# Kernel tuning notes

Hardware: AMD Instinct MI355X
Metric: run time of the kernel (lower is better)

The kernel has to match this reference:

```python
import jax, jax.numpy as jnp
import numpy as np

N = 100000      # n_nodes
D = 64          # in_features (= out_features)
H = 4           # attention heads
DK = D // H     # per-head dim
E = 1600000     # num edges (avg degree 16)
STEP = 0.25     # ODE euler step size
NSTEPS = 4      # integrate t in [0, 1]
ALPHA = 0.2     # LeakyReLU negative slope


def setup_inputs() -> dict:
    key = jax.random.key(0)
    k1, k2, k3, k4 = jax.random.split(key, 4)
    x = jax.random.normal(k1, (N, D), dtype=jnp.float32)
    edge_index = jax.random.randint(k2, (2, E), 0, N, dtype=jnp.int32)
    edge_weight = jax.random.uniform(k3, (E,), dtype=jnp.float32)
    # HamAgg.weight: init.eye_ -> identity [D, D]
    W = jnp.eye(D, dtype=jnp.float32)
    # HAM_GATConv.a: xavier_normal_ on shape (2*d_k, 1, 1), gain=1.414
    a = jax.random.normal(k4, (2 * DK,), dtype=jnp.float32) * (1.414 * np.sqrt(2.0 / (2 * DK + 1)))
    return {"x": x, "edge_index": edge_index, "edge_weight": edge_weight, "W": W, "a": a}


def reference(x, edge_index, edge_weight, W, a):
    # ---- Hamiltonian ODE block (args.vt == 'fc', odemap 'h1extend') ----
    # xt = hstack([x, x @ W.T]); euler-integrate canonical Hamiltonian flow
    # dq/dt = p, dp/dt = -q over t in [0,1] with step 0.25; keep first D dims.
    q = x
    p = x @ W.T
    for _ in range(NSTEPS):
        q, p = q + STEP * p, p - STEP * q
    xt = q  # out_x = out[..., :D]

    row, col = edge_index[0], edge_index[1]

    # ---- HAM_GATConv attention (W_x = x @ I = x) ----
    # h[n, head, k] = xt[n, head*DK + k]
    h = xt.reshape(N, H, DK)
    a_src, a_dst = a[:DK], a[DK:]
    s_src = h @ a_src   # [N, H] per-node source contribution
    s_dst = h @ a_dst   # [N, H] per-node dest contribution
    score = jax.nn.leaky_relu(s_src[row] + s_dst[col], ALPHA)  # [E, H]

    # segment softmax grouped by destination (edge[1])
    seg_max = jax.ops.segment_max(score, col, num_segments=N)  # [N, H]
    seg_max = jnp.where(jnp.isfinite(seg_max), seg_max, 0.0)
    e = jnp.exp(score - seg_max[col])
    denom = jax.ops.segment_sum(e, col, num_segments=N)
    att = e / (denom[col] + 1e-16)  # [E, H]

    # ---- mean over heads of per-head spmm == single spmm with mean attention ----
    # spmm: out[row[e]] += att[e] * xt[col[e]]
    w = att.mean(axis=1)  # [E]
    out = jax.ops.segment_sum(w[:, None] * xt[col], row, num_segments=N)  # [N, D]
    return out
```

## Files before the change

### kernel.cpp

```cpp
#include <hip/hip_runtime.h>
#include <hip/hip_bf16.h>


#define LRELU(v) ((v) > 0.0f ? (v) : 0.2f * (v))

#define EC 4096
#define BSC 256
#define BSR 128
#define NPW 8
#define NPB 32
#define SLOTS 4

__device__ __forceinline__ float bf16_to_f32(unsigned short u) {
    return __uint_as_float((unsigned int)u << 16);
}
__device__ __forceinline__ float bflo(unsigned int u) {
    return __uint_as_float(u << 16);
}
__device__ __forceinline__ float bfhi(unsigned int u) {
    return __uint_as_float(u & 0xFFFF0000u);
}
__device__ __forceinline__ unsigned short f32_to_bf16(float f) {
    __hip_bfloat16 h = __float2bfloat16(f);
    return *reinterpret_cast<unsigned short*>(&h);
}

__global__ __launch_bounds__(256) void k_node(const float* __restrict__ x,
                                              const float* __restrict__ W,
                                              const float* __restrict__ a,
                                              unsigned short* __restrict__ xt16,
                                              float* __restrict__ s_src,
                                              float* __restrict__ s_dst,
                                              int n, float c1, float c2) {
    __shared__ float Ws[64 * 68];
    __shared__ float xs[NPB * 64];
    int t = threadIdx.x;
    for (int i = t; i < 64 * 64; i += 256)
        Ws[(i >> 6) * 68 + (i & 63)] = W[i];
    {
        size_t gbase = (size_t)blockIdx.x * NPB * 64;
        for (int i = t; i < NPB * 64; i += 256) {
            size_t g = gbase + i;
            xs[i] = (g < (size_t)n * 64) ? x[g] : 0.0f;
        }
    }
    __syncthreads();
    int wave = t >> 6;
    int lane = t & 63;
    float a_s = a[lane & 15];
    float a_d = a[16 + (lane & 15)];
    int nbase = blockIdx.x * NPB + wave * NPW;
    const float* xw = xs + wave * NPW * 64;

    float p[NPW];
#pragma unroll
    for (int j = 0; j < NPW; ++j) p[j] = 0.0f;

#pragma unroll 2
    for (int k4 = 0; k4 < 64; k4 += 4) {
        float4 wr = *(const float4*)(Ws + lane * 68 + k4);
#pragma unroll
        for (int j = 0; j < NPW; ++j) {
            float4 xb = *(const float4*)(xw + j * 64 + k4);
            p[j] = fmaf(xb.x, wr.x, p[j]);
            p[j] = fmaf(xb.y, wr.y, p[j]);
            p[j] = fmaf(xb.z, wr.z, p[j]);
            p[j] = fmaf(xb.w, wr.w, p[j]);
        }
    }

#pragma unroll
    for (int j = 0; j < NPW; ++j) {
        int node = nbase + j;
        if (node < n) {
            float xv = xw[j * 64 + lane];
            float xtv = c1 * xv + c2 * p[j];
            xt16[(size_t)node * 64 + lane] = f32_to_bf16(xtv);
            float ss = xtv * a_s;
            float sd = xtv * a_d;
#pragma unroll
            for (int off = 8; off >= 1; off >>= 1) {
                ss += __shfl_xor(ss, off, 64);
                sd += __shfl_xor(sd, off, 64);
            }
            if ((lane & 15) == 0) {
                int h = lane >> 4;
                s_src[node * 4 + h] = ss;
                s_dst[node * 4 + h] = sd;
            }
        }
    }
}

__global__ __launch_bounds__(256) void k_hist(const int* __restrict__ row,
                                              const int* __restrict__ col,
                                              int* __restrict__ Hr,
                                              int* __restrict__ Hc,
                                              int e, int nblk, int nbr, int nbc) {
    __shared__ int hr[1024];
    __shared__ int hc[512];
    int t = threadIdx.x;
    for (int i = t; i < 1024; i += 256) hr[i] = 0;
    for (int i = t; i < 512; i += 256) hc[i] = 0;
    __syncthreads();
    int base = blockIdx.x * EC;
#pragma unroll
    for (int j = 0; j < EC / 256; ++j) {
        int i = base + t + j * 256;
        if (i < e) {
            atomicAdd(&hr[row[i] >> 7], 1);
            atomicAdd(&hc[col[i] >> 8], 1);
        }
    }
    __syncthreads();
    for (int b = t; b < nbr; b += 256) Hr[(size_t)b * nblk + blockIdx.x] = hr[b];
    for (int b = t; b < nbc; b += 256) Hc[(size_t)b * nblk + blockIdx.x] = hc[b];
}

__global__ __launch_bounds__(256) void k_scanH2(int* __restrict__ Hr,
                                                int* __restrict__ Hc,
                                                int* __restrict__ BtotR,
                                                int* __restrict__ BtotC,
                                                int nblk, int nbr) {
    __shared__ int vals[512];
    __shared__ int part[256];
    int t = threadIdx.x;
    int bb = blockIdx.x;
    int* Hb;
    int* Btot;
    if (bb < nbr) {
        Hb = Hr + (size_t)bb * nblk;
        Btot = BtotR + bb;
    } else {
        Hb = Hc + (size_t)(bb - nbr) * nblk;
        Btot = BtotC + (bb - nbr);
    }
    for (int i = t; i < nblk; i += 256) vals[i] = Hb[i];
    __syncthreads();
    int c0 = t * 2;
    int s = 0;
#pragma unroll
    for (int j = 0; j < 2; ++j)
        if (c0 + j < nblk) s += vals[c0 + j];
    part[t] = s;
    __syncthreads();
    for (int d = 1; d < 256; d <<= 1) {
        int add = (t >= d) ? part[t - d] : 0;
        __syncthreads();
        part[t] += add;
        __syncthreads();
    }
    int run = part[t] - s;
#pragma unroll
    for (int j = 0; j < 2; ++j) {
        int i = c0 + j;
        if (i < nblk) {
            int v = vals[i];
            Hb[i] = run;
            run += v;
        }
    }
    if (t == 255) *Btot = part[255];
}

__global__ __launch_bounds__(256) void k_base2(const int* __restrict__ BtotR,
                                               int* __restrict__ BbR, int nbr,
                                               const int* __restrict__ BtotC,
                                               int* __restrict__ BbC, int nbc) {
    const int* Btot = (blockIdx.x == 0) ? BtotR : BtotC;
    int* Bbase = (blockIdx.x == 0) ? BbR : BbC;
    int nb = (blockIdx.x == 0) ? nbr : nbc;
    __shared__ int part[256];
    __shared__ int carry;
    int t = threadIdx.x;
    if (t == 0) carry = 0;
    __syncthreads();
    for (int base = 0; base < nb; base += 256) {
        int i = base + t;
        int v = (i < nb) ? Btot[i] : 0;
        part[t] = v;
        __syncthreads();
        for (int d = 1; d < 256; d <<= 1) {
            int add = (t >= d) ? part[t - d] : 0;
            __syncthreads();
            part[t] += add;
            __syncthreads();
        }
        if (i < nb) Bbase[i] = carry + part[t] - v;
        __syncthreads();
        if (t == 0) carry += part[255];
        __syncthreads();
    }
    if (t == 0) Bbase[nb] = carry;
}

__global__ __launch_bounds__(256) void k_scatter_dual(
    const int* __restrict__ row, const int* __restrict__ col,
    const int* __restrict__ Hr, const int* __restrict__ Hc,
    const int* __restrict__ BbR, const int* __restrict__ BbC,
    int* __restrict__ ebr, int* __restrict__ ebc,
    int e, int nblk, int nbr, int nbc) {
    __shared__ int curr[1024];
    __shared__ int curc[512];
    int t = threadIdx.x;
    int blk = blockIdx.x;
    for (int b = t; b < nbr; b += 256) curr[b] = BbR[b] + Hr[(size_t)b * nblk + blk];
    for (int b = t; b < nbc; b += 256) curc[b] = BbC[b] + Hc[(size_t)b * nblk + blk];
    __syncthreads();
    int base = blk * EC;
#pragma unroll
    for (int j = 0; j < EC / 256; ++j) {
        int i = base + t + j * 256;
        if (i < e) {
            int r = row[i], c = col[i];
            int pr = atomicAdd(&curr[r >> 7], 1);
            ebr[pr] = (c << 7) | (r & 127);
            int pc = atomicAdd(&curc[c >> 8], 1);
            ebc[pc] = (r << 8) | (c & 255);
        }
    }
}

__global__ __launch_bounds__(256) void k_denom_b(const int* __restrict__ ebc,
                                                 const int* __restrict__ BbC,
                                                 const float* __restrict__ s_src,
                                                 const float* __restrict__ s_dst,
                                                 float* __restrict__ rden, int n) {
    __shared__ float acc[BSC * 4];
    __shared__ float sd[BSC * 4];
    int t = threadIdx.x;
    int b = blockIdx.x;
    int cbase = b << 8;
    for (int i = t; i < BSC * 4; i += 256) {
        acc[i] = 0.0f;
        int c4 = cbase * 4 + i;
        sd[i] = (c4 < n * 4) ? s_dst[c4] : 0.0f;
    }
    __syncthreads();
    int start = BbC[b], end = BbC[b + 1];
    for (int i = start + t; i < end; i += 256) {
        int p = ebc[i];
        int r = p >> 8, cl = p & 255;
        float4 ss = *(const float4*)(s_src + (size_t)r * 4);
        atomicAdd(&acc[cl * 4 + 0], __expf(LRELU(ss.x + sd[cl * 4 + 0])));
        atomicAdd(&acc[cl * 4 + 1], __expf(LRELU(ss.y + sd[cl * 4 + 1])));
        atomicAdd(&acc[cl * 4 + 2], __expf(LRELU(ss.z + sd[cl * 4 + 2])));
        atomicAdd(&acc[cl * 4 + 3], __expf(LRELU(ss.w + sd[cl * 4 + 3])));
    }
    __syncthreads();
    for (int i = t; i < BSC * 4; i += 256) {
        int c4 = cbase * 4 + i;
        if (c4 < n * 4) rden[c4] = 1.0f / (acc[i] + 1e-16f);
    }
}

__global__ __launch_bounds__(256) void k_sort2(const int* __restrict__ ebr,
                                               const int* __restrict__ BbR,
                                               const float* __restrict__ s_src,
                                               const float* __restrict__ s_dst,
                                               const float* __restrict__ rden,
                                               int* __restrict__ rowptr,
                                               int2* __restrict__ cwp,
                                               int n, int e) {
    __shared__ int cnt[BSR];
    __shared__ int pfx[BSR];
    __shared__ int cur[BSR];
    __shared__ float ssh[BSR * 4];
    int t = threadIdx.x;
    int b = blockIdx.x;
    int rbase = b << 7;
    if (t < BSR) cnt[t] = 0;
    for (int i = t; i < BSR * 4; i += 256) {
        int g = rbase * 4 + i;
        ssh[i] = (g < n * 4) ? s_src[g] : 0.0f;
    }
    __syncthreads();
    int start = BbR[b], end = BbR[b + 1];
    for (int i = start + t; i < end; i += 256)
        atomicAdd(&cnt[ebr[i] & 127], 1);
    __syncthreads();
    if (t < BSR) pfx[t] = cnt[t];
    __syncthreads();
    for (int d = 1; d < BSR; d <<= 1) {
        int v = (t < BSR && t >= d) ? pfx[t - d] : 0;
        __syncthreads();
        if (t < BSR) pfx[t] += v;
        __syncthreads();
    }
    if (t < BSR) {
        int excl = start + pfx[t] - cnt[t];
        cur[t] = excl;
        int r = rbase + t;
        if (r < n) rowptr[r] = excl;
    }
    if (b == 0 && t == 0) rowptr[n] = e;
    __syncthreads();
    for (int i = start + t; i < end; i += 256) {
        int p = ebr[i];
        int rl = p & 127, c = p >> 7;
        float4 sd = *(const float4*)(s_dst + (size_t)c * 4);
        float4 rd = *(const float4*)(rden + (size_t)c * 4);
        float wv = __expf(LRELU(ssh[rl * 4 + 0] + sd.x)) * rd.x +
                   __expf(LRELU(ssh[rl * 4 + 1] + sd.y)) * rd.y +
                   __expf(LRELU(ssh[rl * 4 + 2] + sd.z)) * rd.z +
                   __expf(LRELU(ssh[rl * 4 + 3] + sd.w)) * rd.w;
        int pos = atomicAdd(&cur[rl], 1);
        cwp[pos] = make_int2(c << 6, __float_as_int(0.25f * wv));
    }
}

__global__ __launch_bounds__(256) void k_aggr(const int* __restrict__ rowptr,
                                              const int2* __restrict__ cwp,
                                              const unsigned short* __restrict__ xt16,
                                              float* __restrict__ out, int n, int e) {
    int r = blockIdx.x * 4 + (threadIdx.x >> 6);
    if (r >= n) return;
    int lane = threadIdx.x & 63;
    int g = lane >> 3;
    unsigned le = (lane & 7) << 3;
    int start = rowptr[r], end = rowptr[r + 1];
    float acc[8];
#pragma unroll
    for (int j = 0; j < 8; ++j) acc[j] = 0.0f;
    for (int base = start; base < end; base += SLOTS * 8) {
        int m = end - base;
        if (m > SLOTS * 8) m = SLOTS * 8;
        int nk = (m + 7) >> 3;
        uint4 u[SLOTS];
        float wv[SLOTS];
#pragma unroll
        for (int k = 0; k < SLOTS; ++k) {
            if (k < nk) {
                int idx = base + k * 8 + g;
                int idc = idx < e ? idx : e - 1;
                int2 cw = cwp[idc];
                wv[k] = (idx < end) ? __int_as_float(cw.y) : 0.0f;
                u[k] = *(const uint4*)(xt16 + ((unsigned)cw.x + le));
            }
        }
#pragma unroll
        for (int k = 0; k < SLOTS; ++k) {
            if (k < nk) {
                acc[0] = fmaf(wv[k], bflo(u[k].x), acc[0]);
                acc[1] = fmaf(wv[k], bfhi(u[k].x), acc[1]);
                acc[2] = fmaf(wv[k], bflo(u[k].y), acc[2]);
                acc[3] = fmaf(wv[k], bfhi(u[k].y), acc[3]);
                acc[4] = fmaf(wv[k], bflo(u[k].z), acc[4]);
                acc[5] = fmaf(wv[k], bfhi(u[k].z), acc[5]);
                acc[6] = fmaf(wv[k], bflo(u[k].w), acc[6]);
                acc[7] = fmaf(wv[k], bfhi(u[k].w), acc[7]);
            }
        }
    }
#pragma unroll
    for (int off = 8; off <= 32; off <<= 1) {
#pragma unroll
        for (int j = 0; j < 8; ++j) acc[j] += __shfl_xor(acc[j], off, 64);
    }
    if (lane < 8) {
        float4 a0 = {acc[0], acc[1], acc[2], acc[3]};
        float4 a1 = {acc[4], acc[5], acc[6], acc[7]};
        *(float4*)(out + (size_t)r * 64 + le) = a0;
        *(float4*)(out + (size_t)r * 64 + le + 4) = a1;
    }
}

extern "C" void kernel_launch(void* const* d_in, const int* in_sizes, int n_in,
                              void* d_out, int out_size, void* d_ws, size_t ws_size,
                              hipStream_t stream) {
    const float* x = (const float*)d_in[0];
    const int* ei = (const int*)d_in[1];
    const float* W = (const float*)d_in[3];
    const float* a = (const float*)d_in[4];
    int n = in_sizes[0] / 64;
    int e = in_sizes[1] / 2;
    const int* row = ei;
    const int* col = ei + e;
    float* out = (float*)d_out;

    int nblk = (e + EC - 1) / EC;
    int nbr = (n + BSR - 1) / BSR;
    int nbc = (n + BSC - 1) / BSC;

    size_t o = 0;
    auto take = [&](size_t cnt) {
        size_t p = o;
        o += (cnt + 3) & ~(size_t)3;
        return p;
    };
    int* wsi = (int*)d_ws;
    unsigned short* xt16 = (unsigned short*)(wsi + take((size_t)n * 32));
    float* s_src = (float*)(wsi + take((size_t)n * 4));
    float* s_dst = (float*)(wsi + take((size_t)n * 4));
    float* rden = (float*)(wsi + take((size_t)n * 4));
    int* Hr = wsi + take((size_t)nbr * nblk);
    int* Hc = wsi + take((size_t)nbc * nblk);
    int* BtotR = wsi + take(nbr);
    int* BbR = wsi + take(nbr + 1);
    int* BtotC = wsi + take(nbc);
    int* BbC = wsi + take(nbc + 1);
    int* ebr = wsi + take(e);
    int* cwbuf = wsi + take((size_t)2 * e);
    int* ebc = cwbuf;
    int2* cwp = (int2*)cwbuf;
    int* rowptr = wsi + take(n + 1);

    float aq = 1.f, bq = 0.f, ap = 0.f, bp = 1.f;
    for (int i = 0; i < 4; ++i) {
        float naq = aq + 0.25f * ap, nbq = bq + 0.25f * bp;
        float nap = ap - 0.25f * aq, nbp = bp - 0.25f * bq;
        aq = naq; bq = nbq; ap = nap; bp = nbp;
    }

    k_node<<<(n + NPB - 1) / NPB, 256, 0, stream>>>(x, W, a, xt16, s_src, s_dst,
                                                    n, aq, bq);
    k_hist<<<nblk, 256, 0, stream>>>(row, col, Hr, Hc, e, nblk, nbr, nbc);
    k_scanH2<<<nbr + nbc, 256, 0, stream>>>(Hr, Hc, BtotR, BtotC, nblk, nbr);
    k_base2<<<2, 256, 0, stream>>>(BtotR, BbR, nbr, BtotC, BbC, nbc);
    k_scatter_dual<<<nblk, 256, 0, stream>>>(row, col, Hr, Hc, BbR, BbC,
                                             ebr, ebc, e, nblk, nbr, nbc);
    k_denom_b<<<nbc, 256, 0, stream>>>(ebc, BbC, s_src, s_dst, rden, n);
    k_sort2<<<nbr, 256, 0, stream>>>(ebr, BbR, s_src, s_dst, rden,
                                     rowptr, cwp, n, e);
    k_aggr<<<(n + 3) / 4, 256, 0, stream>>>(rowptr, cwp, xt16, out, n, e);
}
```

Before: 308.3 us.

## Use bf16 MFMA for node transform and fold attention projections into GEMM

Rewrites the node kernel to compute x@W.T with bf16 MFMA 16x16x32 instructions instead of scalar FMAs out of shared memory. A new one-block kernel precomputes the effective attention projection vectors (W and the ODE coefficients folded into a), split into hi/lo bf16 parts, so s_src and s_dst come out of an extra MFMA tile rather than shuffle reductions. This lowers the node-stage compute and shared-memory cost. In exchange x and W are rounded to bf16 before the matmul, which costs accuracy, and a kernel launch is added.

```diff
diff --git a/kernel.cpp b/kernel.cpp
--- a/kernel.cpp
+++ b/kernel.cpp
@@ -7,9 +7,10 @@
 #define EC 4096
 #define BSC 256
 #define BSR 128
-#define NPW 8
-#define NPB 32
 #define SLOTS 4
+
+typedef __attribute__((ext_vector_type(8))) short bf16x8;
+typedef __attribute__((ext_vector_type(4))) float f32x4;
 
 __device__ __forceinline__ float bf16_to_f32(unsigned short u) {
     return __uint_as_float((unsigned int)u << 16);
@@ -25,69 +26,118 @@
     return *reinterpret_cast<unsigned short*>(&h);
 }
 
+__global__ __launch_bounds__(256) void k_geff(const float* __restrict__ W,
+                                              const float* __restrict__ a,
+                                              unsigned short* __restrict__ geff16,
+                                              float c1, float c2) {
+    int t = threadIdx.x;
+    int k = t & 63, h = t >> 6;
+    float ssrc = 0.0f, sdst = 0.0f;
+#pragma unroll
+    for (int d = 0; d < 16; ++d) {
+        float w = W[(h * 16 + d) * 64 + k];
+        ssrc += w * a[d];
+        sdst += w * a[16 + d];
+    }
+    float gsrc = c2 * ssrc, gdst = c2 * sdst;
+    if ((k >> 4) == h) {
+        gsrc += c1 * a[k & 15];
+        gdst += c1 * a[16 + (k & 15)];
+    }
+    unsigned short sh = f32_to_bf16(gsrc);
+    unsigned short sl = f32_to_bf16(gsrc - bf16_to_f32(sh));
+    unsigned short dh = f32_to_bf16(gdst);
+    unsigned short dl = f32_to_bf16(gdst - bf16_to_f32(dh));
+    geff16[h * 64 + k] = sh;
+    geff16[(4 + h) * 64 + k] = dh;
+    geff16[(8 + h) * 64 + k] = sl;
+    geff16[(12 + h) * 64 + k] = dl;
+}
+
 __global__ __launch_bounds__(256) void k_node(const float* __restrict__ x,
                                               const float* __restrict__ W,
-                                              const float* __restrict__ a,
+                                              const unsigned short* __restrict__ geff16,
                                               unsigned short* __restrict__ xt16,
                                               float* __restrict__ s_src,
                                               float* __restrict__ s_dst,
                                               int n, float c1, float c2) {
-    __shared__ float Ws[64 * 68];
-    __shared__ float xs[NPB * 64];
-    int t = threadIdx.x;
-    for (int i = t; i < 64 * 64; i += 256)
-        Ws[(i >> 6) * 68 + (i & 63)] = W[i];
-    {
-        size_t gbase = (size_t)blockIdx.x * NPB * 64;
-        for (int i = t; i < NPB * 64; i += 256) {
-            size_t g = gbase + i;
-            xs[i] = (g < (size_t)n * 64) ? x[g] : 0.0f;
-        }
-    }
-    __syncthreads();
-    int wave = t >> 6;
-    int lane = t & 63;
-    float a_s = a[lane & 15];
-    float a_d = a[16 + (lane & 15)];
-    int nbase = blockIdx.x * NPB + wave * NPW;
-    const float* xw = xs + wave * NPW * 64;
-
-    float p[NPW];
-#pragma unroll
-    for (int j = 0; j < NPW; ++j) p[j] = 0.0f;
-
-#pragma unroll 2
-    for (int k4 = 0; k4 < 64; k4 += 4) {
-        float4 wr = *(const float4*)(Ws + lane * 68 + k4);
-#pragma unroll
-        for (int j = 0; j < NPW; ++j) {
-            float4 xb = *(const float4*)(xw + j * 64 + k4);
-            p[j] = fmaf(xb.x, wr.x, p[j]);
-            p[j] = fmaf(xb.y, wr.y, p[j]);
-            p[j] = fmaf(xb.z, wr.z, p[j]);
-            p[j] = fmaf(xb.w, wr.w, p[j]);
-        }
-    }
-
-#pragma unroll
-    for (int j = 0; j < NPW; ++j) {
-        int node = nbase + j;
+    int wave = threadIdx.x >> 6;
+    int lane = threadIdx.x & 63;
+    int nb = blockIdx.x * 64 + wave * 16;
+    if (nb >= n) return;
+    int colg = lane & 15;
+    int grp = lane >> 4;
+    int k0 = grp << 3;
+
+    bf16x8 wf[4][2];
+#pragma unroll
+    for (int ct = 0; ct < 4; ++ct) {
+#pragma unroll
+        for (int ks = 0; ks < 2; ++ks) {
+            const float* wr = W + (size_t)(ct * 16 + colg) * 64 + k0 + ks * 32;
+            float4 w0 = *(const float4*)(wr);
+            float4 w1 = *(const float4*)(wr + 4);
+            bf16x8 f;
+            f[0] = (short)f32_to_bf16(w0.x); f[1] = (short)f32_to_bf16(w0.y);
+            f[2] = (short)f32_to_bf16(w0.z); f[3] = (short)f32_to_bf16(w0.w);
+            f[4] = (short)f32_to_bf16(w1.x); f[5] = (short)f32_to_bf16(w1.y);
+            f[6] = (short)f32_to_bf16(w1.z); f[7] = (short)f32_to_bf16(w1.w);
+            wf[ct][ks] = f;
+        }
+    }
+    bf16x8 gf[2];
+#pragma unroll
+    for (int ks = 0; ks < 2; ++ks)
+        gf[ks] = *(const bf16x8*)(geff16 + colg * 64 + k0 + ks * 32);
+
+    int arow = nb + colg;
+    if (arow >= n) arow = n - 1;
+    const float* xr = x + (size_t)arow * 64 + k0;
+    bf16x8 af[2];
+#pragma unroll
+    for (int ks = 0; ks < 2; ++ks) {
+        float4 x0 = *(const float4*)(xr + ks * 32);
+        float4 x1 = *(const float4*)(xr + ks * 32 + 4);
+        bf16x8 f;
+        f[0] = (short)f32_to_bf16(x0.x); f[1] = (short)f32_to_bf16(x0.y);
+        f[2] = (short)f32_to_bf16(x0.z); f[3] = (short)f32_to_bf16(x0.w);
+        f[4] = (short)f32_to_bf16(x1.x); f[5] = (short)f32_to_bf16(x1.y);
+        f[6] = (short)f32_to_bf16(x1.z); f[7] = (short)f32_to_bf16(x1.w);
+        af[ks] = f;
+    }
+
+    f32x4 acc[5];
+#pragma unroll
+    for (int i = 0; i < 5; ++i) acc[i] = (f32x4){0.f, 0.f, 0.f, 0.f};
+#pragma unroll
+    for (int ct = 0; ct < 4; ++ct) {
+        acc[ct] = __builtin_amdgcn_mfma_f32_16x16x32_bf16(af[0], wf[ct][0], acc[ct], 0, 0, 0);
+        acc[ct] = __builtin_amdgcn_mfma_f32_16x16x32_bf16(af[1], wf[ct][1], acc[ct], 0, 0, 0);
+    }
+    acc[4] = __builtin_amdgcn_mfma_f32_16x16x32_bf16(af[0], gf[0], acc[4], 0, 0, 0);
+    acc[4] = __builtin_amdgcn_mfma_f32_16x16x32_bf16(af[1], gf[1], acc[4], 0, 0, 0);
+
+#pragma unroll
+    for (int ct = 0; ct < 4; ++ct) {
+        int col = ct * 16 + colg;
+#pragma unroll
+        for (int rr = 0; rr < 4; ++rr) {
+            int node = nb + grp * 4 + rr;
+            if (node < n) {
+                float xv = x[(size_t)node * 64 + col];
+                float xtv = c1 * xv + c2 * acc[ct][rr];
+                xt16[(size_t)node * 64 + col] = f32_to_bf16(xtv);
+            }
+        }
+    }
+#pragma unroll
+    for (int rr = 0; rr < 4; ++rr) {
+        float v = acc[4][rr];
+        float tot = v + __shfl_xor(v, 8, 64);
+        int node = nb + grp * 4 + rr;
         if (node < n) {
-            float xv = xw[j * 64 + lane];
-            float xtv = c1 * xv + c2 * p[j];
-            xt16[(size_t)node * 64 + lane] = f32_to_bf16(xtv);
-            float ss = xtv * a_s;
-            float sd = xtv * a_d;
-#pragma unroll
-            for (int off = 8; off >= 1; off >>= 1) {
-                ss += __shfl_xor(ss, off, 64);
-                sd += __shfl_xor(sd, off, 64);
-            }
-            if ((lane & 15) == 0) {
-                int h = lane >> 4;
-                s_src[node * 4 + h] = ss;
-                s_dst[node * 4 + h] = sd;
-            }
+            if (colg < 4) s_src[node * 4 + colg] = tot;
+            else if (colg < 8) s_dst[node * 4 + (colg - 4)] = tot;
         }
     }
 }
@@ -393,6 +443,7 @@
     float* s_src = (float*)(wsi + take((size_t)n * 4));
     float* s_dst = (float*)(wsi + take((size_t)n * 4));
     float* rden = (float*)(wsi + take((size_t)n * 4));
+    unsigned short* geff16 = (unsigned short*)(wsi + take(512));
     int* Hr = wsi + take((size_t)nbr * nblk);
     int* Hc = wsi + take((size_t)nbc * nblk);
     int* BtotR = wsi + take(nbr);
@@ -412,8 +463,9 @@
         aq = naq; bq = nbq; ap = nap; bp = nbp;
     }
 
-    k_node<<<(n + NPB - 1) / NPB, 256, 0, stream>>>(x, W, a, xt16, s_src, s_dst,
-                                                    n, aq, bq);
+    k_geff<<<1, 256, 0, stream>>>(W, a, geff16, aq, bq);
+    k_node<<<(n + 63) / 64, 256, 0, stream>>>(x, W, geff16, xt16, s_src, s_dst,
+                                              n, aq, bq);
     k_hist<<<nblk, 256, 0, stream>>>(row, col, Hr, Hc, e, nblk, nbr, nbc);
     k_scanH2<<<nbr + nbc, 256, 0, stream>>>(Hr, Hc, BtotR, BtotC, nblk, nbr);
     k_base2<<<2, 256, 0, stream>>>(BtotR, BbR, nbr, BtotC, BbC, nbc);
```

After: 300.8 us. 1.03x faster.
